# Kernel tuning notes

Hardware: AMD Instinct MI355X
Metric: run time of the kernel (lower is better)

Reference implementation:

```python
import jax, jax.numpy as jnp
import numpy as np

N = 20000   # nodes
E = 320000  # edges (before self-loops)
D = 128     # hidden_dim (= per-head out channels, concat=False)
H = 4       # heads
NEG_SLOPE = 0.2   # GATv2 leaky_relu default
LN_EPS = 1e-5


def setup_inputs() -> dict:
    key = jax.random.key(0)
    ks = jax.random.split(key, 12)
    s = 0.05
    w = lambda k, shp: (jax.random.normal(k, shp, jnp.float32) * s)
    return {
        "x": jax.random.normal(ks[0], (N, D), jnp.float32),
        "src": jax.random.randint(ks[1], (E,), 0, N, jnp.int32),
        "dst": jax.random.randint(ks[2], (E,), 0, N, jnp.int32),
        "Wl1": w(ks[3], (D, H * D)), "Wr1": w(ks[4], (D, H * D)),
        "att1": w(ks[5], (H, D)), "b1": jnp.zeros((D,), jnp.float32),
        "g1": jnp.ones((D,), jnp.float32), "be1": jnp.zeros((D,), jnp.float32),
        "Wl2": w(ks[6], (D, H * D)), "Wr2": w(ks[7], (D, H * D)),
        "att2": w(ks[8], (H, D)), "b2": jnp.zeros((D,), jnp.float32),
        "g2": jnp.ones((D,), jnp.float32), "be2": jnp.zeros((D,), jnp.float32),
    }


def gatv2_conv(x, src, dst, Wl, Wr, att, bias):
    """GATv2Conv with concat=False (mean over heads), share_weights=False."""
    n = x.shape[0]
    xl = (x @ Wl).reshape(n, H, D)  # source-side projection
    xr = (x @ Wr).reshape(n, H, D)  # target-side projection
    m = jax.nn.leaky_relu(xl[src] + xr[dst], NEG_SLOPE)     # [E', H, D]
    e = jnp.einsum('ehd,hd->eh', m, att)                     # [E', H]
    # segment softmax over edges grouped by destination node
    e_max = jax.ops.segment_max(e, dst, num_segments=n)      # [N, H]
    ex = jnp.exp(e - e_max[dst])
    denom = jax.ops.segment_sum(ex, dst, num_segments=n)     # [N, H]
    alpha = ex / (denom[dst] + 1e-16)                        # [E', H]
    out = jax.ops.segment_sum(alpha[:, :, None] * xl[src], dst, num_segments=n)
    return out.mean(axis=1) + bias                           # [N, D]


def layer_norm(x, g, b):
    mu = x.mean(axis=-1, keepdims=True)
    var = ((x - mu) ** 2).mean(axis=-1, keepdims=True)
    return (x - mu) * jax.lax.rsqrt(var + LN_EPS) * g + b


def reference(x, src, dst, Wl1, Wr1, att1, b1, g1, be1,
              Wl2, Wr2, att2, b2, g2, be2):
    n = x.shape[0]
    # PyG GATv2Conv default add_self_loops=True
    loops = jnp.arange(n, dtype=src.dtype)
    s = jnp.concatenate([src, loops])
    d = jnp.concatenate([dst, loops])

    h = gatv2_conv(x, s, d, Wl1, Wr1, att1, b1)
    h = layer_norm(h, g1, be1)
    h = jax.nn.relu(h + x)

    h2 = gatv2_conv(h, s, d, Wl2, Wr2, att2, b2)
    h2 = layer_norm(h2, g2, be2)
    return h2 + h
```

## Files before the change

### kernel.cpp

```cpp
#include <hip/hip_runtime.h>
#include <hip/hip_bf16.h>
#include <hip/hip_fp16.h>

#define NNODES 20000
#define MPAD   20480
#define NEDGES 320000
#define DIM    128
#define NH     4
#define ETOT   (NEDGES + NNODES)
#define LN_EPS 1e-5f

typedef unsigned char  u8;
typedef unsigned short u16;
typedef unsigned int   u32;

typedef _Float16 f16x2 __attribute__((ext_vector_type(2)));
typedef _Float16 f16x8 __attribute__((ext_vector_type(8)));
typedef float    f32x2 __attribute__((ext_vector_type(2)));
typedef float    f32x4 __attribute__((ext_vector_type(4)));

__device__ inline u16 f2h(float f) {
    _Float16 h = (_Float16)f;
    union { _Float16 h; u16 u; } v; v.h = h; return v.u;
}
__device__ inline f16x2 u2h2(u32 u) { union { u32 u; f16x2 h; } v; v.u = u; return v.h; }
__device__ inline u32 h22u(f16x2 h) { union { f16x2 h; u32 u; } v; v.h = h; return v.u; }
__device__ inline f16x2 habs2(f16x2 h) { return u2h2(h22u(h) & 0x7FFF7FFFu); }

#define GLDS16(g, l) __builtin_amdgcn_global_load_lds(                         \
    (const __attribute__((address_space(1))) void*)(g),                        \
    (__attribute__((address_space(3))) void*)(l), 16, 0, 0)


__global__ void k_prep(const float* __restrict__ x, u16* __restrict__ xb,
                       const float* __restrict__ Wl1, const float* __restrict__ Wr1,
                       u16* __restrict__ Bt1,
                       const float* __restrict__ Wl2, const float* __restrict__ Wr2,
                       u16* __restrict__ Bt2,
                       int* __restrict__ deg) {
    int i = blockIdx.x * blockDim.x + threadIdx.x;
    int stride = gridDim.x * blockDim.x;
    if (i < NNODES) deg[i] = 1;
    for (int j = i; j < NNODES * 32; j += stride) {
        float4 v = ((const float4*)x)[j];
        ushort4 o;
        o.x = f2h(v.x); o.y = f2h(v.y); o.z = f2h(v.z); o.w = f2h(v.w);
        ((ushort4*)xb)[j] = o;
    }
    for (int j = i; j < 1024 * 128; j += stride) {
        int n = j >> 7, k = j & 127;
        Bt1[j] = f2h((n < 512) ? Wl1[k * 512 + n] : Wr1[k * 512 + (n - 512)]);
        Bt2[j] = f2h((n < 512) ? Wl2[k * 512 + n] : Wr2[k * 512 + (n - 512)]);
    }
}


__global__ void k_hist(const int* __restrict__ dst, int* __restrict__ deg) {
    int i = blockIdx.x * blockDim.x + threadIdx.x;
    if (i < NEDGES) atomicAdd(&deg[dst[i]], 1);
}

__global__ __launch_bounds__(1024) void k_scan(const int* __restrict__ deg,
                                               int* __restrict__ row,
                                               int* __restrict__ cur) {
    __shared__ int part[1024];
    const int CH = (NNODES + 1023) / 1024;
    int t = threadIdx.x;
    int base = t * CH;
    int s = 0;
    for (int i = 0; i < CH; i++) { int idx = base + i; if (idx < NNODES) s += deg[idx]; }
    part[t] = s;
    __syncthreads();
    for (int off = 1; off < 1024; off <<= 1) {
        int v = (t >= off) ? part[t - off] : 0;
        __syncthreads();
        part[t] += v;
        __syncthreads();
    }
    int run = (t == 0) ? 0 : part[t - 1];
    for (int i = 0; i < CH; i++) {
        int idx = base + i;
        if (idx < NNODES) { row[idx] = run; cur[idx] = run; run += deg[idx]; }
    }
    if (t == 1023) row[NNODES] = part[1023];
}

__global__ void k_scatter(const int* __restrict__ src, const int* __restrict__ dst,
                          int* __restrict__ col, int* __restrict__ cur) {
    int i = blockIdx.x * blockDim.x + threadIdx.x;
    if (i < NEDGES) {
        int d = dst[i];
        int pos = atomicAdd(&cur[d], 1);
        col[pos] = src[i];
    } else if (i < ETOT) {
        int n = i - NEDGES;
        int pos = atomicAdd(&cur[n], 1);
        col[pos] = n;
    }
}


__global__ __launch_bounds__(256, 2) void k_gemm_f16(const u16* __restrict__ A,
                                                     const u16* __restrict__ Bt,
                                                     u16* __restrict__ XL,
                                                     u16* __restrict__ XR) {
    __shared__ u16 smA[128 * 128];
    __shared__ u16 smB[128 * 128];
    const int L   = blockIdx.x;
    const int xcd = L & 7;
    const int w9  = L >> 3;
    const int bm  = (xcd * 20 + (w9 >> 3)) * 128;
    const int bn  = (w9 & 7) * 128;
    const int t  = threadIdx.x;
    const int w  = t >> 6;
    const int l  = t & 63;

    {
        char* smAb = (char*)smA;
        char* smBb = (char*)smB;
#pragma unroll
        for (int p = 0; p < 8; ++p) {
            int rbase = w * 32 + p * 4;
            int row   = rbase + (l >> 4);
            int j     = (l & 15) ^ (row & 7);
            const u16* ga = A  + (size_t)(bm + row) * 128 + j * 8;
            const u16* gb = Bt + (size_t)(bn + row) * 128 + j * 8;
            GLDS16(ga, smAb + rbase * 256);
            GLDS16(gb, smBb + rbase * 256);
        }
    }
    __syncthreads();

    const int wr  = (w >> 1) * 64;
    const int wc  = (w & 1) * 64;
    const int lr  = l & 15;
    const int lkb = (l >> 4) * 16;

    f32x4 acc[4][4] = {};

#pragma unroll
    for (int ks = 0; ks < 4; ++ks) {
        f16x8 af[4], bfr[4];
#pragma unroll
        for (int i = 0; i < 4; ++i) {
            int ra = wr + i * 16 + lr;
            af[i]  = *(const f16x8*)((const char*)smA +
                        ((ra * 256 + ks * 64 + lkb) ^ ((ra & 7) << 4)));
            int rb = wc + i * 16 + lr;
            bfr[i] = *(const f16x8*)((const char*)smB +
                        ((rb * 256 + ks * 64 + lkb) ^ ((rb & 7) << 4)));
        }
#pragma unroll
        for (int mi = 0; mi < 4; ++mi)
#pragma unroll
            for (int ni = 0; ni < 4; ++ni)
                acc[mi][ni] = __builtin_amdgcn_mfma_f32_16x16x32_f16(
                    bfr[ni], af[mi], acc[mi][ni], 0, 0, 0);
    }

    __syncthreads();
    u16* smC = smA;
    {
        const int n4 = (l >> 4) * 4;
#pragma unroll
        for (int mi = 0; mi < 4; ++mi) {
            int m = wr + mi * 16 + lr;
#pragma unroll
            for (int ni = 0; ni < 4; ++ni) {
                int n = wc + ni * 16 + n4;
                f32x4 v = acc[mi][ni];
                ushort4 o;
                o.x = f2h(v[0]); o.y = f2h(v[1]); o.z = f2h(v[2]); o.w = f2h(v[3]);
                *(ushort4*)((char*)smC + (m * 256 + ((n * 2) ^ ((m & 7) << 4)))) = o;
            }
        }
    }
    __syncthreads();
    {
        int r  = t >> 4;
        int cb = (t & 15) * 16;
        const bool left = (bn < 512);
        u16* base = left ? (XL + bn) : (XR + (bn - 512));
#pragma unroll
        for (int p = 0; p < 8; ++p) {
            int row = p * 16 + r;
            uint4 v = *(const uint4*)((const char*)smC +
                        (row * 256 + (cb ^ ((row & 7) << 4))));
            *(uint4*)(base + (size_t)(bm + row) * 512 + (cb >> 1)) = v;
        }
    }
}


__global__ __launch_bounds__(256) void k_attn(const u16* __restrict__ XL,
                                              const u16* __restrict__ XR,
                                              const float* __restrict__ att,
                                              const float* __restrict__ bias,
                                              const float* __restrict__ gamma,
                                              const float* __restrict__ beta,
                                              const int* __restrict__ row,
                                              const int* __restrict__ col,
                                              const float* __restrict__ res,
                                              float* __restrict__ out,
                                              u16* __restrict__ out_h,
                                              int relu_flag) {
    const int wid = __builtin_amdgcn_readfirstlane(threadIdx.x >> 6);
    const int n   = blockIdx.x * 4 + wid;
    const int l   = threadIdx.x & 63;
    const int h   = l >> 4;
    const int e   = l & 15;

    const f16x2 C06 = {(_Float16)0.6f, (_Float16)0.6f};
    const f16x2 C04 = {(_Float16)0.4f, (_Float16)0.4f};

    const size_t lane_off = h * 128 + e * 8;

    uint4 xru = *(const uint4*)(XR + (size_t)n * 512 + lane_off);
    f16x2 xr0 = u2h2(xru.x), xr1 = u2h2(xru.y), xr2 = u2h2(xru.z), xr3 = u2h2(xru.w);

    const float* ap = att + lane_off;
    float4 af0 = *(const float4*)(ap);
    float4 af1 = *(const float4*)(ap + 4);
    f16x2 at0 = {(_Float16)af0.x, (_Float16)af0.y};
    f16x2 at1 = {(_Float16)af0.z, (_Float16)af0.w};
    f16x2 at2 = {(_Float16)af1.x, (_Float16)af1.y};
    f16x2 at3 = {(_Float16)af1.z, (_Float16)af1.w};

    f16x2 acch[4] = {};
    float ssum = 0.f;

    const int beg = row[n], end = row[n + 1];

    int i = beg;
    int j = i + 2;
    {
        int c0 = col[i];
        int c1 = (i + 1 < end) ? col[i + 1] : c0;
        uint4 a0 = *(const uint4*)(XL + (size_t)c0 * 512 + lane_off);
        uint4 a1 = *(const uint4*)(XL + (size_t)c1 * 512 + lane_off);
        bool morej = j < end;
        int d0 = 0, d1 = 0;
        if (morej) { d0 = col[j]; d1 = (j + 1 < end) ? col[j + 1] : d0; }

        while (true) {
            uint4 b0, b1;
            if (morej) {
                b0 = *(const uint4*)(XL + (size_t)d0 * 512 + lane_off);
                b1 = *(const uint4*)(XL + (size_t)d1 * 512 + lane_off);
            }
            int k2 = j + 2;
            bool morek = morej && (k2 < end);
            int e0c = 0, e1c = 0;
            if (morek) { e0c = col[k2]; e1c = (k2 + 1 < end) ? col[k2 + 1] : e0c; }

            bool has2 = (i + 1 < end);
            float e0, e1;
            {
                f16x2 v0 = u2h2(a0.x) + xr0, v1 = u2h2(a0.y) + xr1;
                f16x2 v2 = u2h2(a0.z) + xr2, v3 = u2h2(a0.w) + xr3;
                f16x2 k0 = v0 * C06 + habs2(v0) * C04;
                f16x2 k1 = v1 * C06 + habs2(v1) * C04;
                f16x2 k2h = v2 * C06 + habs2(v2) * C04;
                f16x2 k3 = v3 * C06 + habs2(v3) * C04;
                e0 = __builtin_amdgcn_fdot2(k0, at0, 0.f, false);
                e0 = __builtin_amdgcn_fdot2(k1, at1, e0, false);
                e0 = __builtin_amdgcn_fdot2(k2h, at2, e0, false);
                e0 = __builtin_amdgcn_fdot2(k3, at3, e0, false);
            }
            {
                f16x2 v0 = u2h2(a1.x) + xr0, v1 = u2h2(a1.y) + xr1;
                f16x2 v2 = u2h2(a1.z) + xr2, v3 = u2h2(a1.w) + xr3;
                f16x2 k0 = v0 * C06 + habs2(v0) * C04;
                f16x2 k1 = v1 * C06 + habs2(v1) * C04;
                f16x2 k2h = v2 * C06 + habs2(v2) * C04;
                f16x2 k3 = v3 * C06 + habs2(v3) * C04;
                e1 = __builtin_amdgcn_fdot2(k0, at0, 0.f, false);
                e1 = __builtin_amdgcn_fdot2(k1, at1, e1, false);
                e1 = __builtin_amdgcn_fdot2(k2h, at2, e1, false);
                e1 = __builtin_amdgcn_fdot2(k3, at3, e1, false);
            }
#pragma unroll
            for (int m = 1; m < 16; m <<= 1) {
                e0 += __shfl_xor(e0, m, 64);
                e1 += __shfl_xor(e1, m, 64);
            }
            float p0 = __expf(e0);
            float p1 = has2 ? __expf(e1) : 0.f;
            ssum += p0 + p1;
            _Float16 ph0s = (_Float16)p0, ph1s = (_Float16)p1;
            f16x2 ph0 = {ph0s, ph0s};
            f16x2 ph1 = {ph1s, ph1s};
            acch[0] = acch[0] + ph0 * u2h2(a0.x) + ph1 * u2h2(a1.x);
            acch[1] = acch[1] + ph0 * u2h2(a0.y) + ph1 * u2h2(a1.y);
            acch[2] = acch[2] + ph0 * u2h2(a0.z) + ph1 * u2h2(a1.z);
            acch[3] = acch[3] + ph0 * u2h2(a0.w) + ph1 * u2h2(a1.w);

            if (!morej) break;
            a0 = b0; a1 = b1;
            i = j; j = k2;
            d0 = e0c; d1 = e1c;
            morej = morek;
        }
    }

    float acc[8];
    {
        f32x2 c;
        c = __builtin_convertvector(acch[0], f32x2); acc[0] = c[0]; acc[1] = c[1];
        c = __builtin_convertvector(acch[1], f32x2); acc[2] = c[0]; acc[3] = c[1];
        c = __builtin_convertvector(acch[2], f32x2); acc[4] = c[0]; acc[5] = c[1];
        c = __builtin_convertvector(acch[3], f32x2); acc[6] = c[0]; acc[7] = c[1];
    }
    float inv = 1.f / (ssum + 1e-16f);
#pragma unroll
    for (int jj = 0; jj < 8; ++jj) acc[jj] *= inv;
#pragma unroll
    for (int jj = 0; jj < 8; ++jj) acc[jj] += __shfl_xor(acc[jj], 16, 64);
#pragma unroll
    for (int jj = 0; jj < 8; ++jj) acc[jj] += __shfl_xor(acc[jj], 32, 64);

    if (h == 0) {
        const int dd = e * 8;
        float4 b40 = *(const float4*)(bias + dd);
        float4 b41 = *(const float4*)(bias + dd + 4);
        float y[8];
        y[0] = acc[0]*0.25f + b40.x; y[1] = acc[1]*0.25f + b40.y;
        y[2] = acc[2]*0.25f + b40.z; y[3] = acc[3]*0.25f + b40.w;
        y[4] = acc[4]*0.25f + b41.x; y[5] = acc[5]*0.25f + b41.y;
        y[6] = acc[6]*0.25f + b41.z; y[7] = acc[7]*0.25f + b41.w;

        float s1 = 0.f, s2 = 0.f;
#pragma unroll
        for (int jj = 0; jj < 8; ++jj) { s1 += y[jj]; s2 += y[jj]*y[jj]; }
#pragma unroll
        for (int m = 1; m < 16; m <<= 1) {
            s1 += __shfl_xor(s1, m, 64);
            s2 += __shfl_xor(s2, m, 64);
        }
        float mu = s1 * (1.f / 128.f);
        float var = s2 * (1.f / 128.f) - mu * mu;
        float rstd = rsqrtf(var + LN_EPS);

        float4 g40 = *(const float4*)(gamma + dd);
        float4 g41 = *(const float4*)(gamma + dd + 4);
        float4 e40 = *(const float4*)(beta + dd);
        float4 e41 = *(const float4*)(beta + dd + 4);
        float4 r40 = *(const float4*)(res + (size_t)n * 128 + dd);
        float4 r41 = *(const float4*)(res + (size_t)n * 128 + dd + 4);
        float g[8] = {g40.x,g40.y,g40.z,g40.w,g41.x,g41.y,g41.z,g41.w};
        float be[8] = {e40.x,e40.y,e40.z,e40.w,e41.x,e41.y,e41.z,e41.w};
        float r[8] = {r40.x,r40.y,r40.z,r40.w,r41.x,r41.y,r41.z,r41.w};
#pragma unroll
        for (int jj = 0; jj < 8; ++jj) {
            y[jj] = (y[jj] - mu) * rstd * g[jj] + be[jj] + r[jj];
            if (relu_flag) y[jj] = fmaxf(y[jj], 0.f);
        }
        float4 o0 = {y[0],y[1],y[2],y[3]};
        float4 o1 = {y[4],y[5],y[6],y[7]};
        *(float4*)(out + (size_t)n * 128 + dd)     = o0;
        *(float4*)(out + (size_t)n * 128 + dd + 4) = o1;
        if (out_h) {
            ushort4 oh0, oh1;
            oh0.x = f2h(y[0]); oh0.y = f2h(y[1]); oh0.z = f2h(y[2]); oh0.w = f2h(y[3]);
            oh1.x = f2h(y[4]); oh1.y = f2h(y[5]); oh1.z = f2h(y[6]); oh1.w = f2h(y[7]);
            *(ushort4*)(out_h + (size_t)n * 128 + dd)     = oh0;
            *(ushort4*)(out_h + (size_t)n * 128 + dd + 4) = oh1;
        }
    }
}


extern "C" void kernel_launch(void* const* d_in, const int* in_sizes, int n_in,
                              void* d_out, int out_size, void* d_ws, size_t ws_size,
                              hipStream_t stream) {
    const float* x    = (const float*)d_in[0];
    const int*   src  = (const int*)d_in[1];
    const int*   dst  = (const int*)d_in[2];
    const float* Wl1  = (const float*)d_in[3];
    const float* Wr1  = (const float*)d_in[4];
    const float* att1 = (const float*)d_in[5];
    const float* b1   = (const float*)d_in[6];
    const float* g1   = (const float*)d_in[7];
    const float* be1  = (const float*)d_in[8];
    const float* Wl2  = (const float*)d_in[9];
    const float* Wr2  = (const float*)d_in[10];
    const float* att2 = (const float*)d_in[11];
    const float* b2   = (const float*)d_in[12];
    const float* g2   = (const float*)d_in[13];
    const float* be2  = (const float*)d_in[14];
    float* out = (float*)d_out;

    char* ws = (char*)d_ws;
    size_t off = 0;
    u16*   xlb  = (u16*)(ws + off);   off += (size_t)MPAD * 512 * 2;
    u16*   xrb  = (u16*)(ws + off);   off += (size_t)MPAD * 512 * 2;
    u16*   xb   = (u16*)(ws + off);   off += (size_t)MPAD * 128 * 2;
    float* hbuf = (float*)(ws + off); off += (size_t)NNODES * 128 * 4;
    u16*   Bt1  = (u16*)(ws + off);   off += (size_t)1024 * 128 * 2;
    u16*   Bt2  = (u16*)(ws + off);   off += (size_t)1024 * 128 * 2;
    int*   deg  = (int*)(ws + off);   off += (size_t)NNODES * 4;
    int*   rowp = (int*)(ws + off);   off += (size_t)(NNODES + 1) * 4;
    int*   cur  = (int*)(ws + off);   off += (size_t)NNODES * 4;
    int*   col  = (int*)(ws + off);   off += (size_t)ETOT * 4;

    k_prep<<<1024, 256, 0, stream>>>(x, xb, Wl1, Wr1, Bt1, Wl2, Wr2, Bt2, deg);
    k_hist<<<(NEDGES + 255) / 256, 256, 0, stream>>>(dst, deg);
    k_scan<<<1, 1024, 0, stream>>>(deg, rowp, cur);
    k_scatter<<<(ETOT + 255) / 256, 256, 0, stream>>>(src, dst, col, cur);

    k_gemm_f16<<<MPAD / 128 * 8, 256, 0, stream>>>(xb, Bt1, xlb, xrb);
    k_attn<<<NNODES / 4, 256, 0, stream>>>(xlb, xrb, att1, b1, g1, be1, rowp, col,
                                           x, hbuf, xb , 1);
    k_gemm_f16<<<MPAD / 128 * 8, 256, 0, stream>>>(xb, Bt2, xlb, xrb);
    k_attn<<<NNODES / 4, 256, 0, stream>>>(xlb, xrb, att2, b2, g2, be2, rowp, col,
                                           hbuf, out, (u16*)nullptr, 0);
}
```

Measured before the change: 213.3 us.

## Tile weight transpose via LDS, vectorize scan loads, split attention launches

The weight transpose in k_prep now stages 32x32 tiles through shared memory so both the reads and the writes are coalesced, and the grid is fixed at 256 blocks. k_scan loads degrees as int4 vectors into registers and reuses them for the output pass instead of reading deg twice. Each attention kernel launch is also split into two half-range launches using a node offset. The split adds launch overhead and has no obvious benefit, and the fixed CH=20 with int4 loads depends on exact alignment with NNODES.

```diff
diff --git a/kernel.cpp b/kernel.cpp
--- a/kernel.cpp
+++ b/kernel.cpp
@@ -32,25 +32,45 @@
     (__attribute__((address_space(3))) void*)(l), 16, 0, 0)
 
 
-__global__ void k_prep(const float* __restrict__ x, u16* __restrict__ xb,
+__global__ __launch_bounds__(256) void k_prep(const float* __restrict__ x, u16* __restrict__ xb,
                        const float* __restrict__ Wl1, const float* __restrict__ Wr1,
                        u16* __restrict__ Bt1,
                        const float* __restrict__ Wl2, const float* __restrict__ Wr2,
                        u16* __restrict__ Bt2,
                        int* __restrict__ deg) {
-    int i = blockIdx.x * blockDim.x + threadIdx.x;
-    int stride = gridDim.x * blockDim.x;
-    if (i < NNODES) deg[i] = 1;
-    for (int j = i; j < NNODES * 32; j += stride) {
+    const int b = blockIdx.x, t = threadIdx.x;
+    const int gid = b * 256 + t;
+    if (gid < NNODES) deg[gid] = 1;
+
+    for (int j = gid; j < NNODES * 32; j += 256 * 256) {
         float4 v = ((const float4*)x)[j];
         ushort4 o;
         o.x = f2h(v.x); o.y = f2h(v.y); o.z = f2h(v.z); o.w = f2h(v.w);
         ((ushort4*)xb)[j] = o;
     }
-    for (int j = i; j < 1024 * 128; j += stride) {
-        int n = j >> 7, k = j & 127;
-        Bt1[j] = f2h((n < 512) ? Wl1[k * 512 + n] : Wr1[k * 512 + (n - 512)]);
-        Bt2[j] = f2h((n < 512) ? Wl2[k * 512 + n] : Wr2[k * 512 + (n - 512)]);
+
+    {
+        const int m    = b >> 6;
+        const int tile = b & 63;
+        const int kt   = tile >> 4;
+        const int nt   = tile & 15;
+        const float* W = (m == 0) ? Wl1 : (m == 1) ? Wr1 : (m == 2) ? Wl2 : Wr2;
+        u16* Bt        = (m < 2) ? Bt1 : Bt2;
+        const int nbase = (m & 1) * 512 + nt * 32;
+
+        __shared__ float lds[32][33];
+        const int tx = t & 31, ty = t >> 5;
+#pragma unroll
+        for (int i = 0; i < 4; ++i) {
+            int k = kt * 32 + ty + i * 8;
+            lds[ty + i * 8][tx] = W[k * 512 + nt * 32 + tx];
+        }
+        __syncthreads();
+#pragma unroll
+        for (int i = 0; i < 4; ++i) {
+            int nrow = nbase + ty + i * 8;
+            Bt[nrow * 128 + kt * 32 + tx] = f2h(lds[tx][ty + i * 8]);
+        }
     }
 }
 
@@ -64,11 +84,19 @@
                                                int* __restrict__ row,
                                                int* __restrict__ cur) {
     __shared__ int part[1024];
-    const int CH = (NNODES + 1023) / 1024;
+    const int CH = 20;
     int t = threadIdx.x;
     int base = t * CH;
     int s = 0;
-    for (int i = 0; i < CH; i++) { int idx = base + i; if (idx < NNODES) s += deg[idx]; }
+    int d[20];
+    if (base < NNODES) {
+#pragma unroll
+        for (int q = 0; q < 5; ++q) {
+            int4 v = ((const int4*)(deg + base))[q];
+            d[q*4+0] = v.x; d[q*4+1] = v.y; d[q*4+2] = v.z; d[q*4+3] = v.w;
+            s += v.x + v.y + v.z + v.w;
+        }
+    }
     part[t] = s;
     __syncthreads();
     for (int off = 1; off < 1024; off <<= 1) {
@@ -77,10 +105,12 @@
         part[t] += v;
         __syncthreads();
     }
-    int run = (t == 0) ? 0 : part[t - 1];
-    for (int i = 0; i < CH; i++) {
-        int idx = base + i;
-        if (idx < NNODES) { row[idx] = run; cur[idx] = run; run += deg[idx]; }
+    if (base < NNODES) {
+        int run = (t == 0) ? 0 : part[t - 1];
+#pragma unroll
+        for (int i = 0; i < CH; i++) {
+            row[base + i] = run; cur[base + i] = run; run += d[i];
+        }
     }
     if (t == 1023) row[NNODES] = part[1023];
 }
@@ -203,9 +233,9 @@
                                               const float* __restrict__ res,
                                               float* __restrict__ out,
                                               u16* __restrict__ out_h,
-                                              int relu_flag) {
+                                              int relu_flag, int n0) {
     const int wid = __builtin_amdgcn_readfirstlane(threadIdx.x >> 6);
-    const int n   = blockIdx.x * 4 + wid;
+    const int n   = n0 + blockIdx.x * 4 + wid;
     const int l   = threadIdx.x & 63;
     const int h   = l >> 4;
     const int e   = l & 15;
@@ -403,15 +433,21 @@
     int*   cur  = (int*)(ws + off);   off += (size_t)NNODES * 4;
     int*   col  = (int*)(ws + off);   off += (size_t)ETOT * 4;
 
-    k_prep<<<1024, 256, 0, stream>>>(x, xb, Wl1, Wr1, Bt1, Wl2, Wr2, Bt2, deg);
+    k_prep<<<256, 256, 0, stream>>>(x, xb, Wl1, Wr1, Bt1, Wl2, Wr2, Bt2, deg);
     k_hist<<<(NEDGES + 255) / 256, 256, 0, stream>>>(dst, deg);
     k_scan<<<1, 1024, 0, stream>>>(deg, rowp, cur);
     k_scatter<<<(ETOT + 255) / 256, 256, 0, stream>>>(src, dst, col, cur);
 
+    const int HALF = NNODES / 2;
+
     k_gemm_f16<<<MPAD / 128 * 8, 256, 0, stream>>>(xb, Bt1, xlb, xrb);
-    k_attn<<<NNODES / 4, 256, 0, stream>>>(xlb, xrb, att1, b1, g1, be1, rowp, col,
-                                           x, hbuf, xb , 1);
+    k_attn<<<HALF / 4, 256, 0, stream>>>(xlb, xrb, att1, b1, g1, be1, rowp, col,
+                                         x, hbuf, xb, 1, 0);
+    k_attn<<<HALF / 4, 256, 0, stream>>>(xlb, xrb, att1, b1, g1, be1, rowp, col,
+                                         x, hbuf, xb, 1, HALF);
     k_gemm_f16<<<MPAD / 128 * 8, 256, 0, stream>>>(xb, Bt2, xlb, xrb);
-    k_attn<<<NNODES / 4, 256, 0, stream>>>(xlb, xrb, att2, b2, g2, be2, rowp, col,
-                                           hbuf, out, (u16*)nullptr, 0);
-}
+    k_attn<<<HALF / 4, 256, 0, stream>>>(xlb, xrb, att2, b2, g2, be2, rowp, col,
+                                         hbuf, out, (u16*)nullptr, 0, 0);
+    k_attn<<<HALF / 4, 256, 0, stream>>>(xlb, xrb, att2, b2, g2, be2, rowp, col,
+                                         hbuf, out, (u16*)nullptr, 0, HALF);
+}
```

After: 202.8 us. 4.9% less time.
